# Performance work log

Measured on AMD Instinct MI355X. Metric: run time of the kernel, lower is better.

Reference implementation:

```python
import jax, jax.numpy as jnp
import numpy as np

B, N, D = 4, 2048, 768
H, HD = 12, 64  # heads, head_dim; D == H*HD
SCALE = HD ** -0.5


def setup_inputs() -> dict:
    key = jax.random.key(0)
    k1, k2, k3 = jax.random.split(key, 3)
    x = jax.random.normal(k1, (B, N, D), dtype=jnp.float32)
    w_qkv = jax.random.normal(k2, (D, 3 * D), dtype=jnp.float32) * (D ** -0.5)
    b_qkv = jnp.zeros((3 * D,), dtype=jnp.float32)
    w_proj = jax.random.normal(k3, (D, D), dtype=jnp.float32) * (D ** -0.5)
    b_proj = jnp.zeros((D,), dtype=jnp.float32)
    return {"x": x, "w_qkv": w_qkv, "b_qkv": b_qkv, "w_proj": w_proj, "b_proj": b_proj}


def reference(x, w_qkv, b_qkv, w_proj, b_proj):
    # 1. QKV projection, split into 3
    qkv = x @ w_qkv + b_qkv                      # (B, N, 3D)
    q, k, v = jnp.split(qkv, 3, axis=-1)         # each (B, N, D)
    # 2. reshape to (B, H, N, HD)
    def to_heads(t):
        return t.reshape(B, N, H, HD).transpose(0, 2, 1, 3)
    q, k, v = to_heads(q), to_heads(k), to_heads(v)
    # 3-4. scaled dot-product attention (full score matrix, as in the original)
    scores = jnp.einsum("bhnd,bhmd->bhnm", q, k) * SCALE   # (B, H, N, N)
    attn = jax.nn.softmax(scores, axis=-1)
    # 5. dropout p=0.0 -> identity (eval)
    # 6. weighted sum
    out = jnp.einsum("bhnm,bhmd->bhnd", attn, v)           # (B, H, N, HD)
    # 7. merge heads
    out = out.transpose(0, 2, 1, 3).reshape(B, N, D)
    # 8. output projection
    return out @ w_proj + b_proj
```

## Files before the change

kernel.cpp:

```cpp
#include <hip/hip_runtime.h>
#include <stdint.h>
#include <stddef.h>


typedef __bf16 bf16x8 __attribute__((ext_vector_type(8)));
typedef float  f32x4  __attribute__((ext_vector_type(4)));

__device__ __forceinline__ float bf2f(unsigned short u){
  union { unsigned int i; float f; } x; x.i = ((unsigned int)u) << 16; return x.f;
}
__device__ __forceinline__ unsigned short fast2bf(float f){
  union { float f; unsigned int i; } x; x.f = f;
  return (unsigned short)((x.i + 0x8000u) >> 16);
}
__device__ __forceinline__ unsigned int fbits(float f){
  union { float f; unsigned int i; } x; x.f = f; return x.i;
}
__device__ __forceinline__ unsigned int pk2bf(float lo, float hi){
  unsigned int a = fbits(lo) + 0x8000u;
  unsigned int b = fbits(hi) + 0x8000u;
  return __builtin_amdgcn_perm(b, a, 0x07060302u);
}

#if __has_builtin(__builtin_amdgcn_exp2f)
  #define EXP2F(x) __builtin_amdgcn_exp2f(x)
#else
  #define EXP2F(x) exp2f(x)
#endif

#define GLD16(gp, lp) __builtin_amdgcn_global_load_lds( \
  (__attribute__((address_space(1))) void*)(uintptr_t)(gp), \
  (__attribute__((address_space(3))) void*)(unsigned int)(uintptr_t)(lp), 16, 0, 0)

__global__ void f32_to_bf16(const float* __restrict__ in,
                            unsigned short* __restrict__ out, int n){
  int i = (blockIdx.x * 256 + threadIdx.x) * 4;
  if(i < n){
    float4 v = *(const float4*)(in + i);
    ushort4 o;
    o.x = fast2bf(v.x); o.y = fast2bf(v.y); o.z = fast2bf(v.z); o.w = fast2bf(v.w);
    *(ushort4*)(out + i) = o;
  }
}

__global__ void transpose_f32_bf16(const float* __restrict__ W,
                                   unsigned short* __restrict__ Wt, int K, int N){
  __shared__ float tile[32][33];
  int n0 = blockIdx.x * 32, k0 = blockIdx.y * 32;
  int tx = threadIdx.x, ty = threadIdx.y;
  for(int i = ty; i < 32; i += 8) tile[i][tx] = W[(size_t)(k0 + i) * N + (n0 + tx)];
  __syncthreads();
  for(int i = ty; i < 32; i += 8) Wt[(size_t)(n0 + i) * K + (k0 + tx)] = fast2bf(tile[tx][i]);
}

__global__ __launch_bounds__(256) void transpose_v(const unsigned short* __restrict__ qkv,
                                                   unsigned short* __restrict__ VT){
  __shared__ __align__(16) unsigned short Ts[64*72];
  const int t  = threadIdx.x;
  const int jt = blockIdx.x;
  const int bh = blockIdx.y;
  const int b = bh / 12, h = bh - b*12;
  const unsigned short* src = qkv + (size_t)(b*2048 + jt*64)*2304 + 1536 + h*64;
  #pragma unroll
  for(int c = t; c < 512; c += 256){
    int j = c >> 3, d0 = (c & 7) * 8;
    *(uint4*)&Ts[j*72 + d0] = *(const uint4*)(src + (size_t)j*2304 + d0);
  }
  __syncthreads();
  unsigned short* dst = VT + (size_t)bh*64*2048 + jt*64;
  #pragma unroll
  for(int c = t; c < 512; c += 256){
    int d = c >> 3, j0 = (c & 7) * 8;
    ushort4 lo, hi;
    lo.x = Ts[(j0+0)*72 + d]; lo.y = Ts[(j0+1)*72 + d];
    lo.z = Ts[(j0+2)*72 + d]; lo.w = Ts[(j0+3)*72 + d];
    hi.x = Ts[(j0+4)*72 + d]; hi.y = Ts[(j0+5)*72 + d];
    hi.z = Ts[(j0+6)*72 + d]; hi.w = Ts[(j0+7)*72 + d];
    *(ushort4*)(dst + (size_t)d*2048 + j0)     = lo;
    *(ushort4*)(dst + (size_t)d*2048 + j0 + 4) = hi;
  }
}

template<typename OT>
__global__ __launch_bounds__(256) void gemm_bt(const unsigned short* __restrict__ A,
                                               const unsigned short* __restrict__ Bt,
                                               const float* __restrict__ bias,
                                               OT* __restrict__ C,
                                               int M, int N, int K, int lda){
  __shared__ __align__(16) unsigned short As[2][128*32];
  __shared__ __align__(16) unsigned short Bs[2][128*32];
  const int tid  = threadIdx.x;
  const int lane = tid & 63, w = tid >> 6;
  const int m0 = blockIdx.y * 128, n0 = blockIdx.x * 128;

  f32x4 acc[4][4];
  #pragma unroll
  for(int i=0;i<4;i++)
    #pragma unroll
    for(int j=0;j<4;j++) acc[i][j] = (f32x4){0.f,0.f,0.f,0.f};

  const int c0 = w*64 + lane, c1 = c0 + 256;
  const unsigned short* Ag0 = A  + (size_t)(m0 + (c0>>2)) * lda + (c0&3)*8;
  const unsigned short* Ag1 = A  + (size_t)(m0 + (c1>>2)) * lda + (c1&3)*8;
  const unsigned short* Bg0 = Bt + (size_t)(n0 + (c0>>2)) * K   + (c0&3)*8;
  const unsigned short* Bg1 = Bt + (size_t)(n0 + (c1>>2)) * K   + (c1&3)*8;

  const int wm = w & 1, wn = w >> 1;
  const int quad = lane >> 4, l15 = lane & 15;

  GLD16(Ag0, As[0] +        w*512);
  GLD16(Ag1, As[0] + 2048 + w*512);
  GLD16(Bg0, Bs[0] +        w*512);
  GLD16(Bg1, Bs[0] + 2048 + w*512);

  int cur = 0;
  for(int kt = 0; kt < K; kt += 32){
    __syncthreads();
    if(kt + 32 < K){
      int nx = cur ^ 1;
      GLD16(Ag0 + kt + 32, As[nx] +        w*512);
      GLD16(Ag1 + kt + 32, As[nx] + 2048 + w*512);
      GLD16(Bg0 + kt + 32, Bs[nx] +        w*512);
      GLD16(Bg1 + kt + 32, Bs[nx] + 2048 + w*512);
    }

    bf16x8 af[4], bfr[4];
    #pragma unroll
    for(int mt=0;mt<4;mt++) af[mt]  = *(const bf16x8*)&As[cur][(wm*64 + mt*16 + l15)*32 + quad*8];
    #pragma unroll
    for(int nt=0;nt<4;nt++) bfr[nt] = *(const bf16x8*)&Bs[cur][(wn*64 + nt*16 + l15)*32 + quad*8];
    #pragma unroll
    for(int mt=0;mt<4;mt++)
      #pragma unroll
      for(int nt=0;nt<4;nt++)
        acc[mt][nt] = __builtin_amdgcn_mfma_f32_16x16x32_bf16(af[mt], bfr[nt], acc[mt][nt], 0, 0, 0);
    cur ^= 1;
  }

  #pragma unroll
  for(int nt=0;nt<4;nt++){
    int col = n0 + wn*64 + nt*16 + l15;
    float bv = bias[col];
    #pragma unroll
    for(int mt=0;mt<4;mt++){
      int row0 = m0 + wm*64 + mt*16 + quad*4;
      #pragma unroll
      for(int i=0;i<4;i++){
        float v = acc[mt][nt][i] + bv;
        if constexpr (sizeof(OT) == 2)
          C[(size_t)(row0 + i) * N + col] = (OT)fast2bf(v);
        else
          C[(size_t)(row0 + i) * N + col] = (OT)v;
      }
    }
  }
}

__global__ __launch_bounds__(256, 4) void attn_mfma(unsigned short* __restrict__ qkv,
                                                    const unsigned short* __restrict__ VT){
  __shared__ __align__(16) unsigned short SM[2*64*72];
  __shared__ float lsum_lds[4*64];
  __shared__ float linv_lds[64];

  const int t    = threadIdx.x;
  const int lane = t & 63, w = t >> 6;
  const int quad = lane >> 4, l15 = lane & 15;
  const int b = blockIdx.z, h = blockIdx.y;
  const int i0 = blockIdx.x * 64;

  unsigned short* Qs = SM + 64*72;
  unsigned short* Qg = qkv + (size_t)(b*2048 + i0)*2304 + h*64;

  const float QSCALE = 0.125f * 1.4426950408889634f;
  #pragma unroll
  for(int c = t; c < 512; c += 256){
    int q = c >> 3, d0 = (c & 7) * 8;
    uint4 raw = *(const uint4*)(Qg + (size_t)q*2304 + d0);
    unsigned short* rs = (unsigned short*)&raw;
    ushort4 lo, hi;
    lo.x = fast2bf(bf2f(rs[0])*QSCALE); lo.y = fast2bf(bf2f(rs[1])*QSCALE);
    lo.z = fast2bf(bf2f(rs[2])*QSCALE); lo.w = fast2bf(bf2f(rs[3])*QSCALE);
    hi.x = fast2bf(bf2f(rs[4])*QSCALE); hi.y = fast2bf(bf2f(rs[5])*QSCALE);
    hi.z = fast2bf(bf2f(rs[6])*QSCALE); hi.w = fast2bf(bf2f(rs[7])*QSCALE);
    *(ushort4*)&Qs[q*72 + d0]     = lo;
    *(ushort4*)&Qs[q*72 + d0 + 4] = hi;
  }
  __syncthreads();

  bf16x8 qf[4][2];
  #pragma unroll
  for(int nt=0;nt<4;nt++)
    #pragma unroll
    for(int kc=0;kc<2;kc++)
      qf[nt][kc] = *(const bf16x8*)&Qs[(nt*16 + l15)*72 + kc*32 + quad*8];

  f32x4 oacc[4];
  #pragma unroll
  for(int mt=0;mt<4;mt++) oacc[mt] = (f32x4){0.f,0.f,0.f,0.f};
  float lpart[4] = {0.f,0.f,0.f,0.f};

  const size_t KSTR = (size_t)64*2304;
  const unsigned short* Kp = qkv + (size_t)(b*2048)*2304 + 768 + h*64
                           + (size_t)(w*16 + l15)*2304 + quad*8;
  const unsigned short* Vp = VT + (size_t)(b*12 + h)*64*2048
                           + (size_t)(w*16 + l15)*2048 + quad*8;
  const int prow = (0*16 + l15)*72;

  #define STEP_S(KA0, KA1, DST)                                              \
  {                                                                          \
    f32x4 sacc[4];                                                           \
    _Pragma("unroll")                                                        \
    for(int nt=0;nt<4;nt++) sacc[nt] = (f32x4){0.f,0.f,0.f,0.f};             \
    _Pragma("unroll")                                                        \
    for(int nt=0;nt<4;nt++){                                                 \
      sacc[nt] = __builtin_amdgcn_mfma_f32_16x16x32_bf16(KA0, qf[nt][0], sacc[nt], 0, 0, 0); \
      sacc[nt] = __builtin_amdgcn_mfma_f32_16x16x32_bf16(KA1, qf[nt][1], sacc[nt], 0, 0, 0); \
    }                                                                        \
    _Pragma("unroll")                                                        \
    for(int nt=0;nt<4;nt++){                                                 \
      float p0 = EXP2F(sacc[nt][0]);                                         \
      float p1 = EXP2F(sacc[nt][1]);                                         \
      float p2 = EXP2F(sacc[nt][2]);                                         \
      float p3 = EXP2F(sacc[nt][3]);                                         \
      lpart[nt] += (p0 + p1) + (p2 + p3);                                    \
      uint2 pw; pw.x = pk2bf(p0, p1); pw.y = pk2bf(p2, p3);                  \
      *(uint2*)&(DST)[(nt*16 + l15)*72 + w*16 + quad*4] = pw;                \
    }                                                                        \
  }

  #define STEP_PV(SRC, V0, V1)                                               \
  {                                                                          \
    _Pragma("unroll")                                                        \
    for(int mt=0;mt<4;mt++){                                                 \
      bf16x8 pf0 = *(const bf16x8*)&(SRC)[(mt*16 + l15)*72 + quad*8];        \
      oacc[mt] = __builtin_amdgcn_mfma_f32_16x16x32_bf16(pf0, V0, oacc[mt], 0, 0, 0); \
      bf16x8 pf1 = *(const bf16x8*)&(SRC)[(mt*16 + l15)*72 + 32 + quad*8];   \
      oacc[mt] = __builtin_amdgcn_mfma_f32_16x16x32_bf16(pf1, V1, oacc[mt], 0, 0, 0); \
    }                                                                        \
  }

  unsigned short* P0 = SM;
  unsigned short* P1 = SM + 64*72;

  bf16x8 vA0 = *(const bf16x8*)(Vp);
  bf16x8 vA1 = *(const bf16x8*)(Vp + 32);
  {
    bf16x8 kt0 = *(const bf16x8*)(Kp);
    bf16x8 kt1 = *(const bf16x8*)(Kp + 32);
    STEP_S(kt0, kt1, P0)
  }
  Kp += KSTR;
  bf16x8 kA0 = *(const bf16x8*)(Kp);
  bf16x8 kA1 = *(const bf16x8*)(Kp + 32);
  Kp += KSTR;
  Vp += 64;
  bf16x8 kB0, kB1, vB0, vB1;

  #pragma unroll 1
  for(int it = 0; it < 16; ++it){
    __syncthreads();
    vB0 = *(const bf16x8*)(Vp);
    vB1 = *(const bf16x8*)(Vp + 32);
    Vp += 64;
    if(it < 15){
      kB0 = *(const bf16x8*)(Kp);
      kB1 = *(const bf16x8*)(Kp + 32);
      Kp += KSTR;
    }
    STEP_S(kA0, kA1, P1)
    STEP_PV(P0, vA0, vA1)

    __syncthreads();
    if(it < 15){
      vA0 = *(const bf16x8*)(Vp);
      vA1 = *(const bf16x8*)(Vp + 32);
      Vp += 64;
      kA0 = *(const bf16x8*)(Kp);
      kA1 = *(const bf16x8*)(Kp + 32);
      Kp += KSTR;
      STEP_S(kB0, kB1, P0)
    }
    STEP_PV(P1, vB0, vB1)
  }
  #undef STEP_S
  #undef STEP_PV

  #pragma unroll
  for(int nt=0;nt<4;nt++){
    lpart[nt] += __shfl_xor(lpart[nt], 16, 64);
    lpart[nt] += __shfl_xor(lpart[nt], 32, 64);
  }
  if(quad == 0){
    #pragma unroll
    for(int nt=0;nt<4;nt++) lsum_lds[w*64 + nt*16 + l15] = lpart[nt];
  }
  __syncthreads();
  if(t < 64)
    linv_lds[t] = 1.0f / (lsum_lds[t] + lsum_lds[64+t] + lsum_lds[128+t] + lsum_lds[192+t]);
  __syncthreads();

  #pragma unroll
  for(int mt=0;mt<4;mt++){
    #pragma unroll
    for(int i=0;i<4;i++){
      int q = mt*16 + quad*4 + i;
      float li = linv_lds[q];
      Qg[(size_t)q*2304 + w*16 + l15] = fast2bf(oacc[mt][i] * li);
    }
  }
  (void)prow;
}

extern "C" void kernel_launch(void* const* d_in, const int* in_sizes, int n_in,
                              void* d_out, int out_size, void* d_ws, size_t ws_size,
                              hipStream_t stream){
  const float* x      = (const float*)d_in[0];
  const float* w_qkv  = (const float*)d_in[1];
  const float* b_qkv  = (const float*)d_in[2];
  const float* w_proj = (const float*)d_in[3];
  const float* b_proj = (const float*)d_in[4];
  float* out = (float*)d_out;

  unsigned short* xb      = (unsigned short*)d_ws;
  unsigned short* Wt_qkv  = xb      + (size_t)8192*768;
  unsigned short* Wt_proj = Wt_qkv  + (size_t)2304*768;
  unsigned short* qkvb    = Wt_proj + (size_t)768*768;
  unsigned short* VT      = xb;

  f32_to_bf16<<<(8192*768)/1024, 256, 0, stream>>>(x, xb, 8192*768);
  transpose_f32_bf16<<<dim3(72, 24), dim3(32, 8), 0, stream>>>(w_qkv,  Wt_qkv,  768, 2304);
  transpose_f32_bf16<<<dim3(24, 24), dim3(32, 8), 0, stream>>>(w_proj, Wt_proj, 768, 768);

  gemm_bt<unsigned short><<<dim3(2304/128, 8192/128), 256, 0, stream>>>(
      xb, Wt_qkv, b_qkv, qkvb, 8192, 2304, 768, 768);

  transpose_v<<<dim3(32, 48), 256, 0, stream>>>(qkvb, VT);

  attn_mfma<<<dim3(2048/64, 12, 4), 256, 0, stream>>>(qkvb, VT);

  gemm_bt<float><<<dim3(768/128, 8192/128), 256, 0, stream>>>(
      qkvb, Wt_proj, b_proj, out, 8192, 768, 768, 2304);
}
```

Before: 260.4 us.

## Rewrite attention with 32x32 MFMA and register-resident P via permlane swaps

The attention kernel now gives each wave its own 32 query rows and uses 32x32x16 bf16 MFMAs. The probability tile stays in registers, repacked into the A-operand layout with v_cvt_pk_bf16 and permlane32_swap, so the LDS round trip and the per-iteration block barriers go away. The grid becomes half as many blocks of 128 queries. The cost is that each wave now loads its own K/V tiles with no sharing across waves, the pipeline is less explicit, and occupancy is lowered to 3.

```diff
diff --git a/kernel.cpp b/kernel.cpp
--- a/kernel.cpp
+++ b/kernel.cpp
@@ -5,6 +5,8 @@
 
 typedef __bf16 bf16x8 __attribute__((ext_vector_type(8)));
 typedef float  f32x4  __attribute__((ext_vector_type(4)));
+typedef float  f32x16 __attribute__((ext_vector_type(16)));
+typedef unsigned int u32x2 __attribute__((ext_vector_type(2)));
 
 __device__ __forceinline__ float bf2f(unsigned short u){
   union { unsigned int i; float f; } x; x.i = ((unsigned int)u) << 16; return x.f;
@@ -20,6 +22,19 @@
   unsigned int a = fbits(lo) + 0x8000u;
   unsigned int b = fbits(hi) + 0x8000u;
   return __builtin_amdgcn_perm(b, a, 0x07060302u);
+}
+__device__ __forceinline__ unsigned int cvtpk_bf16(float lo, float hi){
+  unsigned int r;
+  asm("v_cvt_pk_bf16_f32 %0, %1, %2" : "=v"(r) : "v"(lo), "v"(hi));
+  return r;
+}
+__device__ __forceinline__ void plswap32(unsigned int &a, unsigned int &b){
+#if __has_builtin(__builtin_amdgcn_permlane32_swap)
+  u32x2 r = __builtin_amdgcn_permlane32_swap(a, b, false, false);
+  a = r.x; b = r.y;
+#else
+  asm volatile("v_permlane32_swap_b32 %0, %1" : "+v"(a), "+v"(b));
+#endif
 }
 
 #if __has_builtin(__builtin_amdgcn_exp2f)
@@ -156,159 +171,103 @@
   }
 }
 
-__global__ __launch_bounds__(256, 4) void attn_mfma(unsigned short* __restrict__ qkv,
+__global__ __launch_bounds__(256, 3) void attn_mfma(unsigned short* __restrict__ qkv,
                                                     const unsigned short* __restrict__ VT){
-  __shared__ __align__(16) unsigned short SM[2*64*72];
-  __shared__ float lsum_lds[4*64];
-  __shared__ float linv_lds[64];
+  __shared__ float linv_lds[4*32];
 
   const int t    = threadIdx.x;
   const int lane = t & 63, w = t >> 6;
-  const int quad = lane >> 4, l15 = lane & 15;
+  const int l31  = lane & 31, hi = lane >> 5;
   const int b = blockIdx.z, h = blockIdx.y;
-  const int i0 = blockIdx.x * 64;
-
-  unsigned short* Qs = SM + 64*72;
-  unsigned short* Qg = qkv + (size_t)(b*2048 + i0)*2304 + h*64;
+  const int q0 = blockIdx.x * 128 + w * 32;
+
+  unsigned short* Qg = qkv + (size_t)(b*2048 + q0)*2304 + h*64;
 
   const float QSCALE = 0.125f * 1.4426950408889634f;
-  #pragma unroll
-  for(int c = t; c < 512; c += 256){
-    int q = c >> 3, d0 = (c & 7) * 8;
-    uint4 raw = *(const uint4*)(Qg + (size_t)q*2304 + d0);
-    unsigned short* rs = (unsigned short*)&raw;
-    ushort4 lo, hi;
-    lo.x = fast2bf(bf2f(rs[0])*QSCALE); lo.y = fast2bf(bf2f(rs[1])*QSCALE);
-    lo.z = fast2bf(bf2f(rs[2])*QSCALE); lo.w = fast2bf(bf2f(rs[3])*QSCALE);
-    hi.x = fast2bf(bf2f(rs[4])*QSCALE); hi.y = fast2bf(bf2f(rs[5])*QSCALE);
-    hi.z = fast2bf(bf2f(rs[6])*QSCALE); hi.w = fast2bf(bf2f(rs[7])*QSCALE);
-    *(ushort4*)&Qs[q*72 + d0]     = lo;
-    *(ushort4*)&Qs[q*72 + d0 + 4] = hi;
-  }
+  bf16x8 qf[4];
+  #pragma unroll
+  for(int c=0;c<4;c++){
+    uint4 raw = *(const uint4*)(Qg + (size_t)l31*2304 + c*16 + hi*8);
+    const unsigned short* rp = (const unsigned short*)&raw;
+    unsigned short o[8];
+    #pragma unroll
+    for(int e=0;e<8;e++) o[e] = fast2bf(bf2f(rp[e]) * QSCALE);
+    qf[c] = *(const bf16x8*)o;
+  }
+
+  f32x16 oacc0, oacc1;
+  #pragma unroll
+  for(int i=0;i<16;i++){ oacc0[i] = 0.f; oacc1[i] = 0.f; }
+  float lpart = 0.f;
+
+  const size_t KSTEP = (size_t)32*2304;
+  const unsigned short* Kp = qkv + (size_t)(b*2048)*2304 + 768 + h*64
+                           + (size_t)l31*2304 + hi*8;
+  const unsigned short* Vp = VT + (size_t)(b*12 + h)*64*2048
+                           + (size_t)l31*2048 + hi*8;
+
+  bf16x8 kf[4];
+  #pragma unroll
+  for(int c=0;c<4;c++) kf[c] = *(const bf16x8*)(Kp + c*16);
+
+  #pragma unroll 1
+  for(int kt = 0; kt < 2048; kt += 32){
+    f32x16 sacc;
+    #pragma unroll
+    for(int i=0;i<16;i++) sacc[i] = 0.f;
+    sacc = __builtin_amdgcn_mfma_f32_32x32x16_bf16(kf[0], qf[0], sacc, 0, 0, 0);
+    sacc = __builtin_amdgcn_mfma_f32_32x32x16_bf16(kf[1], qf[1], sacc, 0, 0, 0);
+    sacc = __builtin_amdgcn_mfma_f32_32x32x16_bf16(kf[2], qf[2], sacc, 0, 0, 0);
+    sacc = __builtin_amdgcn_mfma_f32_32x32x16_bf16(kf[3], qf[3], sacc, 0, 0, 0);
+
+    bf16x8 vf00 = *(const bf16x8*)(Vp + kt);
+    bf16x8 vf10 = *(const bf16x8*)(Vp + kt + 16);
+    bf16x8 vf01 = *(const bf16x8*)(Vp + kt + (size_t)32*2048);
+    bf16x8 vf11 = *(const bf16x8*)(Vp + kt + (size_t)32*2048 + 16);
+
+    if(kt + 32 < 2048){
+      Kp += KSTEP;
+      #pragma unroll
+      for(int c=0;c<4;c++) kf[c] = *(const bf16x8*)(Kp + c*16);
+    }
+
+    float p[16];
+    #pragma unroll
+    for(int r=0;r<16;r++){ p[r] = EXP2F(sacc[r]); lpart += p[r]; }
+
+    unsigned int d0 = cvtpk_bf16(p[0],  p[1]);
+    unsigned int d1 = cvtpk_bf16(p[2],  p[3]);
+    unsigned int d2 = cvtpk_bf16(p[4],  p[5]);
+    unsigned int d3 = cvtpk_bf16(p[6],  p[7]);
+    unsigned int d4 = cvtpk_bf16(p[8],  p[9]);
+    unsigned int d5 = cvtpk_bf16(p[10], p[11]);
+    unsigned int d6 = cvtpk_bf16(p[12], p[13]);
+    unsigned int d7 = cvtpk_bf16(p[14], p[15]);
+    plswap32(d0, d2); plswap32(d1, d3);
+    plswap32(d4, d6); plswap32(d5, d7);
+    unsigned int c0w[4] = {d0, d1, d2, d3};
+    unsigned int c1w[4] = {d4, d5, d6, d7};
+    bf16x8 pa0 = *(const bf16x8*)c0w;
+    bf16x8 pa1 = *(const bf16x8*)c1w;
+
+    oacc0 = __builtin_amdgcn_mfma_f32_32x32x16_bf16(pa0, vf00, oacc0, 0, 0, 0);
+    oacc1 = __builtin_amdgcn_mfma_f32_32x32x16_bf16(pa0, vf01, oacc1, 0, 0, 0);
+    oacc0 = __builtin_amdgcn_mfma_f32_32x32x16_bf16(pa1, vf10, oacc0, 0, 0, 0);
+    oacc1 = __builtin_amdgcn_mfma_f32_32x32x16_bf16(pa1, vf11, oacc1, 0, 0, 0);
+  }
+
+  lpart += __shfl_xor(lpart, 32, 64);
+  if(lane < 32) linv_lds[w*32 + l31] = 1.0f / lpart;
   __syncthreads();
 
-  bf16x8 qf[4][2];
-  #pragma unroll
-  for(int nt=0;nt<4;nt++)
-    #pragma unroll
-    for(int kc=0;kc<2;kc++)
-      qf[nt][kc] = *(const bf16x8*)&Qs[(nt*16 + l15)*72 + kc*32 + quad*8];
-
-  f32x4 oacc[4];
-  #pragma unroll
-  for(int mt=0;mt<4;mt++) oacc[mt] = (f32x4){0.f,0.f,0.f,0.f};
-  float lpart[4] = {0.f,0.f,0.f,0.f};
-
-  const size_t KSTR = (size_t)64*2304;
-  const unsigned short* Kp = qkv + (size_t)(b*2048)*2304 + 768 + h*64
-                           + (size_t)(w*16 + l15)*2304 + quad*8;
-  const unsigned short* Vp = VT + (size_t)(b*12 + h)*64*2048
-                           + (size_t)(w*16 + l15)*2048 + quad*8;
-  const int prow = (0*16 + l15)*72;
-
-  #define STEP_S(KA0, KA1, DST)                                              \
-  {                                                                          \
-    f32x4 sacc[4];                                                           \
-    _Pragma("unroll")                                                        \
-    for(int nt=0;nt<4;nt++) sacc[nt] = (f32x4){0.f,0.f,0.f,0.f};             \
-    _Pragma("unroll")                                                        \
-    for(int nt=0;nt<4;nt++){                                                 \
-      sacc[nt] = __builtin_amdgcn_mfma_f32_16x16x32_bf16(KA0, qf[nt][0], sacc[nt], 0, 0, 0); \
-      sacc[nt] = __builtin_amdgcn_mfma_f32_16x16x32_bf16(KA1, qf[nt][1], sacc[nt], 0, 0, 0); \
-    }                                                                        \
-    _Pragma("unroll")                                                        \
-    for(int nt=0;nt<4;nt++){                                                 \
-      float p0 = EXP2F(sacc[nt][0]);                                         \
-      float p1 = EXP2F(sacc[nt][1]);                                         \
-      float p2 = EXP2F(sacc[nt][2]);                                         \
-      float p3 = EXP2F(sacc[nt][3]);                                         \
-      lpart[nt] += (p0 + p1) + (p2 + p3);                                    \
-      uint2 pw; pw.x = pk2bf(p0, p1); pw.y = pk2bf(p2, p3);                  \
-      *(uint2*)&(DST)[(nt*16 + l15)*72 + w*16 + quad*4] = pw;                \
-    }                                                                        \
-  }
-
-  #define STEP_PV(SRC, V0, V1)                                               \
-  {                                                                          \
-    _Pragma("unroll")                                                        \
-    for(int mt=0;mt<4;mt++){                                                 \
-      bf16x8 pf0 = *(const bf16x8*)&(SRC)[(mt*16 + l15)*72 + quad*8];        \
-      oacc[mt] = __builtin_amdgcn_mfma_f32_16x16x32_bf16(pf0, V0, oacc[mt], 0, 0, 0); \
-      bf16x8 pf1 = *(const bf16x8*)&(SRC)[(mt*16 + l15)*72 + 32 + quad*8];   \
-      oacc[mt] = __builtin_amdgcn_mfma_f32_16x16x32_bf16(pf1, V1, oacc[mt], 0, 0, 0); \
-    }                                                                        \
-  }
-
-  unsigned short* P0 = SM;
-  unsigned short* P1 = SM + 64*72;
-
-  bf16x8 vA0 = *(const bf16x8*)(Vp);
-  bf16x8 vA1 = *(const bf16x8*)(Vp + 32);
-  {
-    bf16x8 kt0 = *(const bf16x8*)(Kp);
-    bf16x8 kt1 = *(const bf16x8*)(Kp + 32);
-    STEP_S(kt0, kt1, P0)
-  }
-  Kp += KSTR;
-  bf16x8 kA0 = *(const bf16x8*)(Kp);
-  bf16x8 kA1 = *(const bf16x8*)(Kp + 32);
-  Kp += KSTR;
-  Vp += 64;
-  bf16x8 kB0, kB1, vB0, vB1;
-
-  #pragma unroll 1
-  for(int it = 0; it < 16; ++it){
-    __syncthreads();
-    vB0 = *(const bf16x8*)(Vp);
-    vB1 = *(const bf16x8*)(Vp + 32);
-    Vp += 64;
-    if(it < 15){
-      kB0 = *(const bf16x8*)(Kp);
-      kB1 = *(const bf16x8*)(Kp + 32);
-      Kp += KSTR;
-    }
-    STEP_S(kA0, kA1, P1)
-    STEP_PV(P0, vA0, vA1)
-
-    __syncthreads();
-    if(it < 15){
-      vA0 = *(const bf16x8*)(Vp);
-      vA1 = *(const bf16x8*)(Vp + 32);
-      Vp += 64;
-      kA0 = *(const bf16x8*)(Kp);
-      kA1 = *(const bf16x8*)(Kp + 32);
-      Kp += KSTR;
-      STEP_S(kB0, kB1, P0)
-    }
-    STEP_PV(P1, vB0, vB1)
-  }
-  #undef STEP_S
-  #undef STEP_PV
-
-  #pragma unroll
-  for(int nt=0;nt<4;nt++){
-    lpart[nt] += __shfl_xor(lpart[nt], 16, 64);
-    lpart[nt] += __shfl_xor(lpart[nt], 32, 64);
-  }
-  if(quad == 0){
-    #pragma unroll
-    for(int nt=0;nt<4;nt++) lsum_lds[w*64 + nt*16 + l15] = lpart[nt];
-  }
-  __syncthreads();
-  if(t < 64)
-    linv_lds[t] = 1.0f / (lsum_lds[t] + lsum_lds[64+t] + lsum_lds[128+t] + lsum_lds[192+t]);
-  __syncthreads();
-
-  #pragma unroll
-  for(int mt=0;mt<4;mt++){
-    #pragma unroll
-    for(int i=0;i<4;i++){
-      int q = mt*16 + quad*4 + i;
-      float li = linv_lds[q];
-      Qg[(size_t)q*2304 + w*16 + l15] = fast2bf(oacc[mt][i] * li);
-    }
-  }
-  (void)prow;
+  #pragma unroll
+  for(int r=0;r<16;r++){
+    int qrow = (r&3) + 8*(r>>2) + 4*hi;
+    float li = linv_lds[w*32 + qrow];
+    unsigned short* row = Qg + (size_t)qrow*2304;
+    row[l31]      = fast2bf(oacc0[r] * li);
+    row[32 + l31] = fast2bf(oacc1[r] * li);
+  }
 }
 
 extern "C" void kernel_launch(void* const* d_in, const int* in_sizes, int n_in,
@@ -336,7 +295,7 @@
 
   transpose_v<<<dim3(32, 48), 256, 0, stream>>>(qkvb, VT);
 
-  attn_mfma<<<dim3(2048/64, 12, 4), 256, 0, stream>>>(qkvb, VT);
+  attn_mfma<<<dim3(2048/128, 12, 4), 256, 0, stream>>>(qkvb, VT);
 
   gemm_bt<float><<<dim3(768/128, 8192/128), 256, 0, stream>>>(
       qkvb, Wt_proj, b_proj, out, 8192, 768, 768, 2304);
```

Measured after the change: 335.6 us. 28.9% more time.
